# Optimization experiments

Hardware: AMD Instinct MI355X
Metric: run time of the kernel (lower is better)

Reference implementation:

```python
import jax, jax.numpy as jnp
import numpy as np

ATT_HEAD = 12
IN_DIM = 768
OUT_DIM = IN_DIM // ATT_HEAD
LEAKY_ALPHA = 0.2
B, N = 8, 512


def setup_inputs() -> dict:
    key = jax.random.key(0)
    ks = jax.random.split(key, 8)
    feat_in = jax.random.normal(ks[0], (B, N, IN_DIM), dtype=jnp.float32)
    adj = jax.random.randint(ks[1], (B, N, N), 0, 2) > 0
    # xavier_uniform for W: fan_in=in_dim, fan_out=out_dim
    lim_W = float(np.sqrt(6.0 / (IN_DIM + OUT_DIM)))
    W = jax.random.uniform(ks[2], (ATT_HEAD, IN_DIM, OUT_DIM), minval=-lim_W, maxval=lim_W, dtype=jnp.float32)
    b = jnp.zeros((OUT_DIM,), dtype=jnp.float32)
    lim_w = float(np.sqrt(6.0 / (OUT_DIM + 1)))
    w_src = jax.random.uniform(ks[3], (ATT_HEAD, OUT_DIM, 1), minval=-lim_w, maxval=lim_w, dtype=jnp.float32)
    w_dst = jax.random.uniform(ks[4], (ATT_HEAD, OUT_DIM, 1), minval=-lim_w, maxval=lim_w, dtype=jnp.float32)
    # xavier_normal for H.weight [in_dim, in_dim]
    std_H = float(np.sqrt(2.0 / (IN_DIM + IN_DIM)))
    H_w = jax.random.normal(ks[5], (IN_DIM, IN_DIM), dtype=jnp.float32) * std_H
    H_b = jax.random.normal(ks[6], (IN_DIM,), dtype=jnp.float32) * 0.01
    return {"feat_in": feat_in, "adj": adj, "W": W, "b": b,
            "w_src": w_src, "w_dst": w_dst, "H_w": H_w, "H_b": H_b}


def reference(feat_in, adj, W, b, w_src, w_dst, H_w, H_b):
    # h: [B, heads, N, out_dim]
    h = jnp.einsum('bnd,ade->bane', feat_in, W)
    th = jnp.tanh(h)
    attn_src = jnp.einsum('bane,aeo->bano', th, w_src)  # [B,A,N,1]
    attn_dst = jnp.einsum('bane,aeo->bano', th, w_dst)  # [B,A,N,1]
    attn = attn_src + jnp.swapaxes(attn_dst, 2, 3)      # [B,A,N,N]
    attn = jnp.where(attn >= 0, attn, LEAKY_ALPHA * attn)
    mask = ~adj[:, None, :, :]                           # [B,1,N,N]
    attn = jnp.where(mask, jnp.float32(-999.0), attn)
    attn = jax.nn.softmax(attn, axis=-1)
    feat_out = jnp.einsum('banm,bame->bane', attn, h) + b
    feat_out = jnp.swapaxes(feat_out, 1, 2).reshape(feat_in.shape[0], feat_in.shape[1], -1)
    feat_out = jax.nn.elu(feat_out)
    gate = jax.nn.sigmoid(feat_in @ H_w.T + H_b)
    return gate * feat_out + (1.0 - gate) * feat_in
```

## Files before the change

### kernel.cpp

```cpp
#include <hip/hip_runtime.h>
#include <hip/hip_bf16.h>
#include <hip/hip_fp16.h>

#define BB 8
#define NN 512
#define AH 12
#define DIN 768
#define EE 64
#define MM (BB*NN)
#define YY (BB*AH)
#define LEAKY 0.2f

typedef unsigned short u16;
typedef unsigned int u32;
typedef __attribute__((ext_vector_type(8))) short short8;
typedef __attribute__((ext_vector_type(4))) float f32x4;
typedef __attribute__((ext_vector_type(4))) u32 u32x4;
typedef __attribute__((ext_vector_type(4))) u16 u16x4;
typedef __attribute__((ext_vector_type(4))) _Float16 h16x4;

static __device__ __forceinline__ u16 f2bf(float f) {
    u32 u = __builtin_bit_cast(u32, f);
    u32 r = (u + 0x7FFFu + ((u >> 16) & 1u)) >> 16;
    return (u16)r;
}
static __device__ __forceinline__ u32 pk2(float a, float b) {
    return (u32)f2bf(a) | ((u32)f2bf(b) << 16);
}
static __device__ __forceinline__ u32 cvtpk(float a, float b) {
    u32 r;
    asm("v_cvt_pk_bf16_f32 %0, %1, %2" : "=v"(r) : "v"(a), "v"(b));
    return r;
}
static __device__ __forceinline__ float ftanh(float x) {
    x = fminf(fmaxf(x, -15.f), 15.f);
    return 1.f - 2.f / (__expf(2.f * x) + 1.f);
}
static __device__ __forceinline__ float sigm(float z) {
    z = fminf(fmaxf(z, -80.f), 80.f);
    return 1.f / (1.f + __expf(-z));
}
static __device__ __forceinline__ void gl_lds16(const u16* g, u16* l) {
    __builtin_amdgcn_global_load_lds((const __attribute__((address_space(1))) unsigned int*)g,
                                     (__attribute__((address_space(3))) unsigned int*)l,
                                     16, 0, 0);
}

static __device__ __forceinline__ void mfma_probe(int lane, int* prow, int* pcol) {
    int q = lane >> 4, x = lane & 15;
    short8 af, bf;
#pragma unroll
    for (int j = 0; j < 8; j++) {
        int k = q * 8 + j;
        af[j] = (short)f2bf((k < 16) ? (float)(x * 16 + k) : 0.f);
        bf[j] = (short)f2bf((k == x) ? 1.f : 0.f);
    }
    f32x4 d = {};
    d = __builtin_amdgcn_mfma_f32_16x16x32_bf16(af, bf, d, 0, 0, 0);
#pragma unroll
    for (int r = 0; r < 4; r++) {
        int v = (int)(d[r] + 0.5f);
        prow[r] = v >> 4;
        pcol[r] = v & 15;
    }
}

#define N_FEAT (MM*DIN)
#define N_W    (AH*DIN*EE)
#define PACK_BLOCKS (MM/4)
#define FEATV_BLOCKS (N_FEAT/1024)
#define HWBV_BLOCKS (N_W/1024)
#define WT_BLOCKS (AH*(DIN/64))
#define PREP_BLOCKS (PACK_BLOCKS + FEATV_BLOCKS + HWBV_BLOCKS + WT_BLOCKS)

__global__ __launch_bounds__(256) void prep_kernel(const int* __restrict__ adj,
                                                   const float* __restrict__ feat,
                                                   const float* __restrict__ W,
                                                   const float* __restrict__ Hw,
                                                   u32* __restrict__ maskbuf,
                                                   u16* __restrict__ featb,
                                                   u16* __restrict__ Wt,
                                                   u16* __restrict__ Hwb) {
    int blk = blockIdx.x, t = threadIdx.x;
    if (blk < PACK_BLOCKS) {
        int w = t >> 6, ln = t & 63;
        int row = blk * 4 + w;
        const int* ar = adj + (size_t)row * NN;
#pragma unroll
        for (int it = 0; it < 8; it++) {
            unsigned long long bal = __ballot(ar[it * 64 + ln] != 0);
            if (ln == 0) {
                maskbuf[row * 16 + it * 2]     = (u32)bal;
                maskbuf[row * 16 + it * 2 + 1] = (u32)(bal >> 32);
            }
        }
        return;
    }
    blk -= PACK_BLOCKS;
    if (blk < FEATV_BLOCKS) {
        int i = blk * 1024 + t * 4;
        float4 v = *(const float4*)&feat[i];
        u16x4 o = { f2bf(v.x), f2bf(v.y), f2bf(v.z), f2bf(v.w) };
        *(u16x4*)&featb[i] = o;
        return;
    }
    blk -= FEATV_BLOCKS;
    if (blk < HWBV_BLOCKS) {
        int i = blk * 1024 + t * 4;
        float4 v = *(const float4*)&Hw[i];
        u16x4 o = { f2bf(v.x), f2bf(v.y), f2bf(v.z), f2bf(v.w) };
        *(u16x4*)&Hwb[i] = o;
        return;
    }
    blk -= HWBV_BLOCKS;
    __shared__ float tile[64][65];
    int a = blk / (DIN / 64), d0 = (blk % (DIN / 64)) * 64;
    int rl = t >> 4, c4 = (t & 15) * 4;
#pragma unroll
    for (int i = 0; i < 4; i++) {
        int dl = i * 16 + rl;
        float4 v = *(const float4*)&W[((size_t)a * DIN + d0 + dl) * EE + c4];
        tile[dl][c4 + 0] = v.x;
        tile[dl][c4 + 1] = v.y;
        tile[dl][c4 + 2] = v.z;
        tile[dl][c4 + 3] = v.w;
    }
    __syncthreads();
#pragma unroll
    for (int i = 0; i < 4; i++) {
        int e = i * 16 + rl;
        u16x4 o = { f2bf(tile[c4 + 0][e]), f2bf(tile[c4 + 1][e]),
                    f2bf(tile[c4 + 2][e]), f2bf(tile[c4 + 3][e]) };
        *(u16x4*)&Wt[(size_t)a * EE * DIN + (size_t)e * DIN + d0 + c4] = o;
    }
}

__global__ __launch_bounds__(256) void gemm_fused_kernel(const u16* __restrict__ featb,
                                                         const u16* __restrict__ Wt,
                                                         const u16* __restrict__ Hwb,
                                                         const float* __restrict__ wsrc,
                                                         const float* __restrict__ wdst,
                                                         const float* __restrict__ Hb,
                                                         u16* __restrict__ hT,
                                                         float2* __restrict__ Spair,
                                                         float2* __restrict__ Dpair,
                                                         _Float16* __restrict__ Gbuf) {
    __shared__ alignas(16) char smem[49152];
    u16* As0 = (u16*)smem;
    u16* BW0 = (u16*)(smem + 8192);
    u16* BG0 = (u16*)(smem + 16384);
    u16* As1 = (u16*)(smem + 24576);
    u16* BW1 = (u16*)(smem + 32768);
    u16* BG1 = (u16*)(smem + 40960);
    float (*cs)[68] = (float (*)[68])smem;

    int t = threadIdx.x, w = t >> 6, lane = t & 63, q = lane >> 4, x = lane & 15;
    int m0 = blockIdx.x * 64, a = blockIdx.y;

    int wm = w & 1, wn = w >> 1, xr = x & 7;
    int srow = t >> 3;
    int skoff = ((t & 7) ^ (srow & 7)) * 8;
    const u16* Agp  = featb + (size_t)m0 * DIN + srow * DIN + skoff;
    const u16* BWgp = Wt + (size_t)a * EE * DIN + srow * DIN + skoff;
    const u16* BGgp = Hwb + (size_t)(a * EE) * DIN + srow * DIN + skoff;
    int wo = w * 512;
    f32x4 aW00 = {}, aW01 = {}, aW10 = {}, aW11 = {};
    f32x4 aG00 = {}, aG01 = {}, aG10 = {}, aG11 = {};

#define STAGE(A_, BW_, BG_, K_)                                   \
    do {                                                          \
        gl_lds16(Agp + (K_), (A_) + wo);                          \
        gl_lds16(Agp + 32 * DIN + (K_), (A_) + wo + 2048);        \
        gl_lds16(BWgp + (K_), (BW_) + wo);                        \
        gl_lds16(BWgp + 32 * DIN + (K_), (BW_) + wo + 2048);      \
        gl_lds16(BGgp + (K_), (BG_) + wo);                        \
        gl_lds16(BGgp + 32 * DIN + (K_), (BG_) + wo + 2048);      \
    } while (0)

#define COMPUTE(A_, BW_, BG_)                                                       \
    do {                                                                            \
        const u16* ApA  = (A_)  + (wm * 32 + x) * 64;                               \
        const u16* ApBW = (BW_) + (wn * 32 + x) * 64;                               \
        const u16* ApBG = (BG_) + (wn * 32 + x) * 64;                               \
        _Pragma("unroll")                                                           \
        for (int kk = 0; kk < 2; kk++) {                                            \
            int c8 = ((q + kk * 4) ^ xr) * 8;                                       \
            short8 a0 = *(const short8*)(ApA + c8);                                 \
            short8 a1 = *(const short8*)(ApA + 16 * 64 + c8);                       \
            short8 bW0 = *(const short8*)(ApBW + c8);                               \
            short8 bW1 = *(const short8*)(ApBW + 16 * 64 + c8);                     \
            short8 bG0 = *(const short8*)(ApBG + c8);                               \
            short8 bG1 = *(const short8*)(ApBG + 16 * 64 + c8);                     \
            aW00 = __builtin_amdgcn_mfma_f32_16x16x32_bf16(a0, bW0, aW00, 0, 0, 0); \
            aW01 = __builtin_amdgcn_mfma_f32_16x16x32_bf16(a0, bW1, aW01, 0, 0, 0); \
            aW10 = __builtin_amdgcn_mfma_f32_16x16x32_bf16(a1, bW0, aW10, 0, 0, 0); \
            aW11 = __builtin_amdgcn_mfma_f32_16x16x32_bf16(a1, bW1, aW11, 0, 0, 0); \
            aG00 = __builtin_amdgcn_mfma_f32_16x16x32_bf16(a0, bG0, aG00, 0, 0, 0); \
            aG01 = __builtin_amdgcn_mfma_f32_16x16x32_bf16(a0, bG1, aG01, 0, 0, 0); \
            aG10 = __builtin_amdgcn_mfma_f32_16x16x32_bf16(a1, bG0, aG10, 0, 0, 0); \
            aG11 = __builtin_amdgcn_mfma_f32_16x16x32_bf16(a1, bG1, aG11, 0, 0, 0); \
        }                                                                           \
    } while (0)

    STAGE(As0, BW0, BG0, 0);
    __syncthreads();
#pragma unroll 1
    for (int k0 = 0; k0 < DIN; k0 += 128) {
        STAGE(As1, BW1, BG1, k0 + 64);
        COMPUTE(As0, BW0, BG0);
        __syncthreads();
        if (k0 + 128 < DIN) STAGE(As0, BW0, BG0, k0 + 128);
        COMPUTE(As1, BW1, BG1);
        __syncthreads();
    }
#undef STAGE
#undef COMPUTE

    int prow[4], pcol[4];
    mfma_probe(lane, prow, pcol);

#pragma unroll
    for (int r = 0; r < 4; r++) {
        cs[wm * 32 + prow[r]][wn * 32 + pcol[r]]           = aW00[r];
        cs[wm * 32 + prow[r]][wn * 32 + 16 + pcol[r]]      = aW01[r];
        cs[wm * 32 + 16 + prow[r]][wn * 32 + pcol[r]]      = aW10[r];
        cs[wm * 32 + 16 + prow[r]][wn * 32 + 16 + pcol[r]] = aW11[r];
    }
    __syncthreads();

    int b = m0 >> 9;
    int y = b * AH + a;
    int nbase = m0 & 511;
    {
        int kcb = nbase >> 3;
#pragma unroll
        for (int i = 0; i < 2; i++) {
            int idx = i * 256 + t;
            int kcl = idx >> 6, e = idx & 63;
            int r0 = kcl * 8;
            u32x4 wv = { pk2(cs[r0 + 0][e], cs[r0 + 1][e]),
                         pk2(cs[r0 + 2][e], cs[r0 + 3][e]),
                         pk2(cs[r0 + 4][e], cs[r0 + 5][e]),
                         pk2(cs[r0 + 6][e], cs[r0 + 7][e]) };
            *(u32x4*)&hT[((((size_t)y << 6) + kcb + kcl) << 6 | e) * 8] = wv;
        }
    }
    {
        int r = t >> 2, cg = t & 3;
        float s = 0.f, d = 0.f;
#pragma unroll
        for (int i = 0; i < 16; i++) {
            int e2 = cg * 16 + i;
            float th = ftanh(cs[r][e2]);
            s += th * wsrc[a * EE + e2];
            d += th * wdst[a * EE + e2];
        }
        s += __shfl_xor(s, 1); s += __shfl_xor(s, 2);
        d += __shfl_xor(d, 1); d += __shfl_xor(d, 2);
        if (cg == 0) {
            s = fminf(fmaxf(s, -40.f), 40.f);
            d = fminf(fmaxf(d, -40.f), 40.f);
            Spair[y * NN + nbase + r] = make_float2(__expf(s), __expf(0.2f * s));
            Dpair[y * NN + nbase + r] = make_float2(__expf(d), __expf(0.2f * d));
        }
    }
    __syncthreads();

#pragma unroll
    for (int r = 0; r < 4; r++) {
        cs[wm * 32 + prow[r]][wn * 32 + pcol[r]]           = aG00[r];
        cs[wm * 32 + prow[r]][wn * 32 + 16 + pcol[r]]      = aG01[r];
        cs[wm * 32 + 16 + prow[r]][wn * 32 + pcol[r]]      = aG10[r];
        cs[wm * 32 + 16 + prow[r]][wn * 32 + 16 + pcol[r]] = aG11[r];
    }
    __syncthreads();

    {
        int n0 = a * EE;
        float4 hb = *(const float4*)&Hb[n0 + (t & 15) * 4];
#pragma unroll
        for (int p = 0; p < 4; p++) {
            int ml = p * 16 + (t >> 4), c4 = (t & 15) * 4;
            float4 v4 = *(const float4*)&cs[ml][c4];
            size_t idx = (size_t)(m0 + ml) * DIN + n0 + c4;
            h16x4 o = { (_Float16)sigm(v4.x + hb.x),
                        (_Float16)sigm(v4.y + hb.y),
                        (_Float16)sigm(v4.z + hb.z),
                        (_Float16)sigm(v4.w + hb.w) };
            *(h16x4*)&Gbuf[idx] = o;
        }
    }
}

__global__ __launch_bounds__(256) void attn_kernel(const u16* __restrict__ hT,
                                                   const float2* __restrict__ Spair,
                                                   const float2* __restrict__ Dpair,
                                                   const u32* __restrict__ maskbuf,
                                                   const float* __restrict__ bias,
                                                   const _Float16* __restrict__ Gbuf,
                                                   const float* __restrict__ feat,
                                                   float* __restrict__ out) {
    __shared__ alignas(16) float2 sd2[NN];
    __shared__ u32 smask[64][17];
    __shared__ float silv[64];
    __shared__ alignas(16) float cs[64][68];
    __shared__ alignas(16) u16 Hs[2][2048];

    int t = threadIdx.x;
    int y = blockIdx.y, bb = y / AH, a = y % AH;
    int i0 = blockIdx.x * 64;
    int w = t >> 6, lane = t & 63, q = lane >> 4, x = lane & 15;

    sd2[t] = Dpair[y * NN + t];
    sd2[t + 256] = Dpair[y * NN + 256 + t];
#pragma unroll
    for (int p = 0; p < 4; p++) {
        int idx = p * 256 + t, r = idx >> 4, c = idx & 15;
        smask[r][c] = maskbuf[((bb << 9) + i0 + r) * 16 + c];
    }

    const u16* hTy = hT + ((size_t)y << 12) * 8;
    const u16* gstage = hTy + t * 8;
    u16* lstage = &Hs[0][0] + w * 512;

    gl_lds16(gstage, lstage);
    __syncthreads();

    int rowl = w * 16 + x;
    float2 se = Spair[y * NN + i0 + rowl];
    float es1 = se.x, es2 = se.y;

    u32 anym = 0;
#pragma unroll
    for (int c = 0; c < 16; c++) anym |= smask[rowl][c];
    int uni = (anym == 0);

    f32x4 acc[4] = {};
    float lsum = 0.f;

#pragma unroll 2
    for (int k0 = 0; k0 < NN; k0 += 32) {
        int cur = (k0 >> 5) & 1;
        if (k0 + 32 < NN)
            gl_lds16(gstage + ((k0 + 32) >> 3) * 512, &Hs[cur ^ 1][0] + w * 512);

        u32 mb = smask[rowl][k0 >> 5] >> (q * 8);
        const float4* sdp = (const float4*)&sd2[k0 + q * 8];
        float pv[8];
#pragma unroll
        for (int jj = 0; jj < 4; jj++) {
            float4 d4 = sdp[jj];
            float p0 = fmaxf(es1 * d4.x, es2 * d4.y);
            float p1 = fmaxf(es1 * d4.z, es2 * d4.w);
            p0 = ((mb >> (2 * jj)) & 1) ? p0 : 0.f;
            p1 = ((mb >> (2 * jj + 1)) & 1) ? p1 : 0.f;
            p0 = uni ? 1.0f : p0;
            p1 = uni ? 1.0f : p1;
            lsum += p0 + p1;
            pv[2 * jj] = p0;
            pv[2 * jj + 1] = p1;
        }
        short8 af = __builtin_bit_cast(short8, (u32x4){
            cvtpk(pv[0], pv[1]), cvtpk(pv[2], pv[3]),
            cvtpk(pv[4], pv[5]), cvtpk(pv[6], pv[7])});
        const u16* hp = &Hs[cur][0] + (q * 64 + x) * 8;
        short8 b0 = *(const short8*)(hp);
        short8 b1 = *(const short8*)(hp + 128);
        short8 b2 = *(const short8*)(hp + 256);
        short8 b3 = *(const short8*)(hp + 384);
        acc[0] = __builtin_amdgcn_mfma_f32_16x16x32_bf16(af, b0, acc[0], 0, 0, 0);
        acc[1] = __builtin_amdgcn_mfma_f32_16x16x32_bf16(af, b1, acc[1], 0, 0, 0);
        acc[2] = __builtin_amdgcn_mfma_f32_16x16x32_bf16(af, b2, acc[2], 0, 0, 0);
        acc[3] = __builtin_amdgcn_mfma_f32_16x16x32_bf16(af, b3, acc[3], 0, 0, 0);
        __syncthreads();
    }

    lsum += __shfl_xor(lsum, 16);
    lsum += __shfl_xor(lsum, 32);
    if (q == 0) silv[rowl] = 1.f / fmaxf(lsum, 1e-30f);

    int prow[4], pcol[4];
    mfma_probe(lane, prow, pcol);
#pragma unroll
    for (int nt = 0; nt < 4; nt++)
#pragma unroll
        for (int r = 0; r < 4; r++)
            cs[w * 16 + prow[r]][nt * 16 + pcol[r]] = acc[nt][r];
    __syncthreads();

    float4 b4 = *(const float4*)&bias[(t & 15) * 4];
#pragma unroll
    for (int p = 0; p < 4; p++) {
        int nl = p * 16 + (t >> 4), e4 = (t & 15) * 4;
        float il = silv[nl];
        float4 c4 = *(const float4*)&cs[nl][e4];
        size_t base = ((size_t)(bb << 9) + i0 + nl) * DIN + a * EE + e4;
        h16x4 g4 = *(const h16x4*)&Gbuf[base];
        float4 f4 = *(const float4*)&feat[base];
        float4 o;
        float v, e, g;
        v = c4.x * il + b4.x; e = v > 0.f ? v : __expf(v) - 1.f; g = (float)g4.x; o.x = g * e + (1.f - g) * f4.x;
        v = c4.y * il + b4.y; e = v > 0.f ? v : __expf(v) - 1.f; g = (float)g4.y; o.y = g * e + (1.f - g) * f4.y;
        v = c4.z * il + b4.z; e = v > 0.f ? v : __expf(v) - 1.f; g = (float)g4.z; o.z = g * e + (1.f - g) * f4.z;
        v = c4.w * il + b4.w; e = v > 0.f ? v : __expf(v) - 1.f; g = (float)g4.w; o.w = g * e + (1.f - g) * f4.w;
        *(float4*)&out[base] = o;
    }
}

extern "C" void kernel_launch(void* const* d_in, const int* in_sizes, int n_in,
                              void* d_out, int out_size, void* d_ws, size_t ws_size,
                              hipStream_t stream) {
    const float* feat  = (const float*)d_in[0];
    const int*   adj   = (const int*)  d_in[1];
    const float* W     = (const float*)d_in[2];
    const float* bvec  = (const float*)d_in[3];
    const float* wsrc  = (const float*)d_in[4];
    const float* wdst  = (const float*)d_in[5];
    const float* Hw    = (const float*)d_in[6];
    const float* Hb    = (const float*)d_in[7];
    float* out = (float*)d_out;

    char* ws = (char*)d_ws;
    u16*    featb   = (u16*)(ws);
    u16*    Wt      = (u16*)(ws + 6291456);
    u16*    Hwb     = (u16*)(ws + 7471104);
    u16*    hT      = (u16*)(ws + 8650752);
    float2* Spair   = (float2*)(ws + 14942208);
    float2* Dpair   = (float2*)(ws + 15335424);
    u32*    maskbuf = (u32*)(ws + 15728640);
    _Float16* Gbuf  = (_Float16*)(ws + 15990784);

    prep_kernel<<<PREP_BLOCKS, 256, 0, stream>>>(
        adj, feat, W, Hw, maskbuf, featb, Wt, Hwb);
    gemm_fused_kernel<<<dim3(MM / 64, AH), 256, 0, stream>>>(
        featb, Wt, Hwb, wsrc, wdst, Hb, hT, Spair, Dpair, Gbuf);
    attn_kernel<<<dim3(NN / 64, YY), 256, 0, stream>>>(
        hT, Spair, Dpair, maskbuf, bvec, Gbuf, feat, out);
}
```

Before: 118.7 us.

## Fuse fp32-to-bf16 feature conversion into GEMM A-tile staging and prefetch epilogue loads

The separate prep pass that converts feat to bf16 is removed. The GEMM now loads fp32 feat rows into registers, converts them to bf16 and writes them into LDS, overlapped with the B-tile async copies and the MFMA compute. This drops one full read and write of a bf16 copy of the features plus its workspace. The attention kernel also issues its epilogue loads of the gate and feat values early, so they overlap with the attention loop, at the cost of extra registers and twice the global A traffic per GEMM tile, since fp32 is re-read by every head block.

```diff
diff --git a/kernel.cpp b/kernel.cpp
--- a/kernel.cpp
+++ b/kernel.cpp
@@ -65,20 +65,16 @@
     }
 }
 
-#define N_FEAT (MM*DIN)
 #define N_W    (AH*DIN*EE)
 #define PACK_BLOCKS (MM/4)
-#define FEATV_BLOCKS (N_FEAT/1024)
-#define HWBV_BLOCKS (N_W/1024)
+#define HWBV_BLOCKS ((DIN*DIN)/1024)
 #define WT_BLOCKS (AH*(DIN/64))
-#define PREP_BLOCKS (PACK_BLOCKS + FEATV_BLOCKS + HWBV_BLOCKS + WT_BLOCKS)
+#define PREP_BLOCKS (PACK_BLOCKS + HWBV_BLOCKS + WT_BLOCKS)
 
 __global__ __launch_bounds__(256) void prep_kernel(const int* __restrict__ adj,
-                                                   const float* __restrict__ feat,
                                                    const float* __restrict__ W,
                                                    const float* __restrict__ Hw,
                                                    u32* __restrict__ maskbuf,
-                                                   u16* __restrict__ featb,
                                                    u16* __restrict__ Wt,
                                                    u16* __restrict__ Hwb) {
     int blk = blockIdx.x, t = threadIdx.x;
@@ -97,14 +93,6 @@
         return;
     }
     blk -= PACK_BLOCKS;
-    if (blk < FEATV_BLOCKS) {
-        int i = blk * 1024 + t * 4;
-        float4 v = *(const float4*)&feat[i];
-        u16x4 o = { f2bf(v.x), f2bf(v.y), f2bf(v.z), f2bf(v.w) };
-        *(u16x4*)&featb[i] = o;
-        return;
-    }
-    blk -= FEATV_BLOCKS;
     if (blk < HWBV_BLOCKS) {
         int i = blk * 1024 + t * 4;
         float4 v = *(const float4*)&Hw[i];
@@ -135,7 +123,7 @@
     }
 }
 
-__global__ __launch_bounds__(256) void gemm_fused_kernel(const u16* __restrict__ featb,
+__global__ __launch_bounds__(256) void gemm_fused_kernel(const float* __restrict__ featf,
                                                          const u16* __restrict__ Wt,
                                                          const u16* __restrict__ Hwb,
                                                          const float* __restrict__ wsrc,
@@ -160,17 +148,36 @@
     int wm = w & 1, wn = w >> 1, xr = x & 7;
     int srow = t >> 3;
     int skoff = ((t & 7) ^ (srow & 7)) * 8;
-    const u16* Agp  = featb + (size_t)m0 * DIN + srow * DIN + skoff;
+    const float* Afp = featf + (size_t)(m0 + srow) * DIN + skoff;
     const u16* BWgp = Wt + (size_t)a * EE * DIN + srow * DIN + skoff;
     const u16* BGgp = Hwb + (size_t)(a * EE) * DIN + srow * DIN + skoff;
     int wo = w * 512;
     f32x4 aW00 = {}, aW01 = {}, aW10 = {}, aW11 = {};
     f32x4 aG00 = {}, aG01 = {}, aG10 = {}, aG11 = {};
-
-#define STAGE(A_, BW_, BG_, K_)                                   \
+    float4 av0, av1, av2, av3;
+
+#define A_LOAD(K_)                                                \
     do {                                                          \
-        gl_lds16(Agp + (K_), (A_) + wo);                          \
-        gl_lds16(Agp + 32 * DIN + (K_), (A_) + wo + 2048);        \
+        const float* ap = Afp + (K_);                             \
+        av0 = *(const float4*)ap;                                 \
+        av1 = *(const float4*)(ap + 4);                           \
+        const float* ap2 = ap + 32 * DIN;                         \
+        av2 = *(const float4*)ap2;                                \
+        av3 = *(const float4*)(ap2 + 4);                          \
+    } while (0)
+
+#define A_WRITE(A_)                                                           \
+    do {                                                                      \
+        u32x4 w0 = { cvtpk(av0.x, av0.y), cvtpk(av0.z, av0.w),                \
+                     cvtpk(av1.x, av1.y), cvtpk(av1.z, av1.w) };              \
+        u32x4 w1 = { cvtpk(av2.x, av2.y), cvtpk(av2.z, av2.w),                \
+                     cvtpk(av3.x, av3.y), cvtpk(av3.z, av3.w) };              \
+        *(u32x4*)((A_) + t * 8) = w0;                                         \
+        *(u32x4*)((A_) + 2048 + t * 8) = w1;                                  \
+    } while (0)
+
+#define STAGE_B(BW_, BG_, K_)                                     \
+    do {                                                          \
         gl_lds16(BWgp + (K_), (BW_) + wo);                        \
         gl_lds16(BWgp + 32 * DIN + (K_), (BW_) + wo + 2048);      \
         gl_lds16(BGgp + (K_), (BG_) + wo);                        \
@@ -202,18 +209,28 @@
         }                                                                           \
     } while (0)
 
-    STAGE(As0, BW0, BG0, 0);
+    A_LOAD(0);
+    STAGE_B(BW0, BG0, 0);
+    A_WRITE(As0);
     __syncthreads();
 #pragma unroll 1
     for (int k0 = 0; k0 < DIN; k0 += 128) {
-        STAGE(As1, BW1, BG1, k0 + 64);
+        A_LOAD(k0 + 64);
+        STAGE_B(BW1, BG1, k0 + 64);
         COMPUTE(As0, BW0, BG0);
+        A_WRITE(As1);
         __syncthreads();
-        if (k0 + 128 < DIN) STAGE(As0, BW0, BG0, k0 + 128);
+        if (k0 + 128 < DIN) {
+            A_LOAD(k0 + 128);
+            STAGE_B(BW0, BG0, k0 + 128);
+        }
         COMPUTE(As1, BW1, BG1);
+        if (k0 + 128 < DIN) A_WRITE(As0);
         __syncthreads();
     }
-#undef STAGE
+#undef A_LOAD
+#undef A_WRITE
+#undef STAGE_B
 #undef COMPUTE
 
     int prow[4], pcol[4];
@@ -319,6 +336,17 @@
         smask[r][c] = maskbuf[((bb << 9) + i0 + r) * 16 + c];
     }
 
+    float4 f4p[4];
+    h16x4 g4p[4];
+    size_t ebase[4];
+#pragma unroll
+    for (int p = 0; p < 4; p++) {
+        int nl = p * 16 + (t >> 4), e4 = (t & 15) * 4;
+        ebase[p] = ((size_t)(bb << 9) + i0 + nl) * DIN + a * EE + e4;
+        g4p[p] = *(const h16x4*)&Gbuf[ebase[p]];
+        f4p[p] = *(const float4*)&feat[ebase[p]];
+    }
+
     const u16* hTy = hT + ((size_t)y << 12) * 8;
     const u16* gstage = hTy + t * 8;
     u16* lstage = &Hs[0][0] + w * 512;
@@ -394,16 +422,15 @@
         int nl = p * 16 + (t >> 4), e4 = (t & 15) * 4;
         float il = silv[nl];
         float4 c4 = *(const float4*)&cs[nl][e4];
-        size_t base = ((size_t)(bb << 9) + i0 + nl) * DIN + a * EE + e4;
-        h16x4 g4 = *(const h16x4*)&Gbuf[base];
-        float4 f4 = *(const float4*)&feat[base];
+        h16x4 g4 = g4p[p];
+        float4 f4 = f4p[p];
         float4 o;
         float v, e, g;
         v = c4.x * il + b4.x; e = v > 0.f ? v : __expf(v) - 1.f; g = (float)g4.x; o.x = g * e + (1.f - g) * f4.x;
         v = c4.y * il + b4.y; e = v > 0.f ? v : __expf(v) - 1.f; g = (float)g4.y; o.y = g * e + (1.f - g) * f4.y;
         v = c4.z * il + b4.z; e = v > 0.f ? v : __expf(v) - 1.f; g = (float)g4.z; o.z = g * e + (1.f - g) * f4.z;
         v = c4.w * il + b4.w; e = v > 0.f ? v : __expf(v) - 1.f; g = (float)g4.w; o.w = g * e + (1.f - g) * f4.w;
-        *(float4*)&out[base] = o;
+        *(float4*)&out[ebase[p]] = o;
     }
 }
 
@@ -421,19 +448,18 @@
     float* out = (float*)d_out;
 
     char* ws = (char*)d_ws;
-    u16*    featb   = (u16*)(ws);
-    u16*    Wt      = (u16*)(ws + 6291456);
-    u16*    Hwb     = (u16*)(ws + 7471104);
-    u16*    hT      = (u16*)(ws + 8650752);
-    float2* Spair   = (float2*)(ws + 14942208);
-    float2* Dpair   = (float2*)(ws + 15335424);
-    u32*    maskbuf = (u32*)(ws + 15728640);
-    _Float16* Gbuf  = (_Float16*)(ws + 15990784);
+    u16*    Wt      = (u16*)(ws);
+    u16*    Hwb     = (u16*)(ws + 1179648);
+    u16*    hT      = (u16*)(ws + 2359296);
+    float2* Spair   = (float2*)(ws + 8650752);
+    float2* Dpair   = (float2*)(ws + 9043968);
+    u32*    maskbuf = (u32*)(ws + 9437184);
+    _Float16* Gbuf  = (_Float16*)(ws + 9699328);
 
     prep_kernel<<<PREP_BLOCKS, 256, 0, stream>>>(
-        adj, feat, W, Hw, maskbuf, featb, Wt, Hwb);
+        adj, W, Hw, maskbuf, Wt, Hwb);
     gemm_fused_kernel<<<dim3(MM / 64, AH), 256, 0, stream>>>(
-        featb, Wt, Hwb, wsrc, wdst, Hb, hT, Spair, Dpair, Gbuf);
+        feat, Wt, Hwb, wsrc, wdst, Hb, hT, Spair, Dpair, Gbuf);
     attn_kernel<<<dim3(NN / 64, YY), 256, 0, stream>>>(
         hT, Spair, Dpair, maskbuf, bvec, Gbuf, feat, out);
 }
```

Result: slower. 121.0 us (+2.0%).
